# Performance work log

Measured on AMD Instinct MI355X. Metric: run time of the kernel, lower is better.

The kernel has to match this reference:

```python
import jax, jax.numpy as jnp
import numpy as np


def setup_inputs() -> dict:
    key = jax.random.key(0)
    ks = jax.random.split(key, 4)
    B, C, H, W = 4, 512, 64, 64
    A = 512  # attention_dim
    x = jax.random.normal(ks[0], (B, C, H, W), dtype=jnp.float32)
    # 1x1 conv weights as [out_ch, in_ch] matrices (kaiming-like scale)
    scale = np.sqrt(2.0 / C).astype(np.float32)
    Wq = jax.random.normal(ks[1], (A, C), dtype=jnp.float32) * scale
    Wk = jax.random.normal(ks[2], (A, C), dtype=jnp.float32) * scale
    Wv = jax.random.normal(ks[3], (C, C), dtype=jnp.float32) * scale
    bq = jnp.zeros((A,), dtype=jnp.float32)
    bk = jnp.zeros((A,), dtype=jnp.float32)
    bv = jnp.zeros((C,), dtype=jnp.float32)
    return {"x": x, "Wq": Wq, "bq": bq, "Wk": Wk, "bk": bk, "Wv": Wv, "bv": bv}


def reference(x, Wq, bq, Wk, bk, Wv, bv):
    B, C, H, W = x.shape
    N = H * W
    xf = x.reshape(B, C, N)  # [B, C, N]
    # 1x1 convs == per-pixel channel matmuls
    q = jnp.einsum('ac,bcn->bna', Wq, xf) + bq[None, None, :]   # [B, N, A] (query, permuted)
    k = jnp.einsum('ac,bcn->ban', Wk, xf) + bk[None, :, None]   # [B, A, N] (key)
    v = jnp.einsum('oc,bcn->bno', Wv, xf) + bv[None, None, :]   # [B, N, C] (value, permuted)
    attn = jnp.einsum('bna,bam->bnm', q, k)                     # [B, N, N]
    attn = jax.nn.softmax(attn, axis=-2)                        # softmax over dim=-2 (queries)
    out = jnp.einsum('bnm,bmc->bnc', attn, v)                   # [B, N, C]
    # Faithful to torch: .view(B, C, H, W) reinterprets the [B, N, C] buffer
    out = out.reshape(B, C, H, W)
    return x + 0.1 * out
```

## Files before the change

kernel.cpp:

```cpp
#include <hip/hip_runtime.h>
#include <stdint.h>


#define LDT 40
#define SUB 5120

typedef _Float16 f16x8 __attribute__((ext_vector_type(8)));
typedef float f32x4 __attribute__((ext_vector_type(4)));

template <int ASRC, int EPI, int NSUB>
__global__ void __launch_bounds__(256, 2) gemm_f16(
    const _Float16* __restrict__ Ap, long lda, long zsa,
    const _Float16* __restrict__ Bp, long ldb, long zsb,
    int kslice,
    const _Float16* __restrict__ fs16, long zsl,
    float* __restrict__ outF, _Float16* __restrict__ outH, long ldc, long zso,
    const float* __restrict__ bias0, const float* __restrict__ bias1,
    const float* __restrict__ xadd,
    float* __restrict__ pmax, float* __restrict__ psum, long zsp,
    float alpha)
{
  __shared__ _Float16 smem[2 * NSUB * SUB];

  const int z = blockIdx.z;
  const long i0 = (long)blockIdx.x * 128;
  const long j0 = (long)blockIdx.y * 128;
  const int t = (int)threadIdx.x;
  const int lane = t & 63;
  const int wv = t >> 6;
  const int quad = lane >> 4;
  const int lrow = lane & 15;
  const int wm = (wv & 1) << 6;
  const int wn = (wv >> 1) << 6;

  const int r0 = t >> 2;
  const int s0 = (t & 3) << 3;

  const _Float16* gA0 = Ap + z * zsa + (i0 + r0) * lda + s0;
  const _Float16* gA1 = gA0 + 64 * lda;
  const _Float16* gB0 = Bp + z * zsb + (j0 + r0) * ldb + s0;
  const _Float16* gB1 = gB0 + 64 * ldb;
  const int la0 = r0 * LDT + s0;
  const int la1 = (r0 + 64) * LDT + s0;

  const _Float16* fsZ = nullptr;
  if constexpr (ASRC == 1)
    fsZ = fs16 + z * zsl + (long)blockIdx.x * 4096 + s0;

  f32x4 acc[4][4];
  const f32x4 fz = {0.f, 0.f, 0.f, 0.f};
#pragma unroll
  for (int a = 0; a < 4; a++)
#pragma unroll
    for (int b = 0; b < 4; b++) acc[a][b] = fz;

  for (int kk = 0; kk < kslice; kk += 32 * NSUB) {
    f16x8 va[NSUB][2], vb[NSUB][2];
#pragma unroll
    for (int s = 0; s < NSUB; s++) {
      va[s][0] = *(const f16x8*)(gA0 + kk + 32 * s);
      va[s][1] = *(const f16x8*)(gA1 + kk + 32 * s);
      vb[s][0] = *(const f16x8*)(gB0 + kk + 32 * s);
      vb[s][1] = *(const f16x8*)(gB1 + kk + 32 * s);
    }
    if constexpr (ASRC == 1) {
#pragma unroll
      for (int s = 0; s < NSUB; s++) {
        const f16x8 fsv = *(const f16x8*)(fsZ + kk + 32 * s);
        va[s][0] = va[s][0] * fsv;
        va[s][1] = va[s][1] * fsv;
      }
    }
    __syncthreads();
#pragma unroll
    for (int s = 0; s < NSUB; s++) {
      *(f16x8*)&smem[s * SUB + la0] = va[s][0];
      *(f16x8*)&smem[s * SUB + la1] = va[s][1];
      *(f16x8*)&smem[(NSUB + s) * SUB + la0] = vb[s][0];
      *(f16x8*)&smem[(NSUB + s) * SUB + la1] = vb[s][1];
    }
    __syncthreads();

#pragma unroll
    for (int h = 0; h < NSUB; h++) {
      const _Float16* pA = smem + h * SUB;
      const _Float16* pB = smem + (NSUB + h) * SUB;
      f16x8 fa[4], fb[4];
#pragma unroll
      for (int f = 0; f < 4; f++) {
        fa[f] = *(const f16x8*)&pA[(wm + f * 16 + lrow) * LDT + quad * 8];
        fb[f] = *(const f16x8*)&pB[(wn + f * 16 + lrow) * LDT + quad * 8];
      }
#pragma unroll
      for (int fm = 0; fm < 4; fm++)
#pragma unroll
        for (int fn = 0; fn < 4; fn++)
          acc[fm][fn] = __builtin_amdgcn_mfma_f32_16x16x32_f16(fa[fm], fb[fn], acc[fm][fn], 0, 0, 0);
    }
  }

  const long obase = (long)z * zso;

  if constexpr (EPI == 1 || EPI == 2) {
#pragma unroll
    for (int fm = 0; fm < 4; fm++) {
      const long gi0 = i0 + wm + fm * 16 + quad * 4;
#pragma unroll
      for (int fn = 0; fn < 4; fn++) {
        const long gj = j0 + wn + fn * 16 + lrow;
        float badd = 0.f;
        if constexpr (EPI == 1) badd = (gj < 512) ? bias0[gj] : bias1[gj - 512];
#pragma unroll
        for (int r = 0; r < 4; r++) {
          float v = acc[fm][fn][r];
          if constexpr (EPI == 1) v += badd;
          else v += bias0[gi0 + r];
          outH[obase + (gi0 + r) * ldc + gj] = (_Float16)v;
        }
      }
    }
  } else if constexpr (EPI == 3) {
#pragma unroll
    for (int fm = 0; fm < 4; fm++) {
      const long gi0 = i0 + wm + fm * 16 + quad * 4;
#pragma unroll
      for (int fn = 0; fn < 4; fn++) {
        const long gj = j0 + wn + fn * 16 + lrow;
#pragma unroll
        for (int r = 0; r < 4; r++) {
          const long o = obase + (gi0 + r) * ldc + gj;
          outF[o] = fmaf(alpha, acc[fm][fn][r], xadd[o]);
        }
      }
    }
  } else {
    __syncthreads();
    float* Ls = (float*)smem;
#pragma unroll
    for (int fn = 0; fn < 4; fn++) {
      float mx = -3.4e38f;
#pragma unroll
      for (int fm = 0; fm < 4; fm++)
#pragma unroll
        for (int r = 0; r < 4; r++) mx = fmaxf(mx, acc[fm][fn][r]);
      Ls[(wv * 4 + quad) * 64 + fn * 16 + lrow] = mx;
    }
    __syncthreads();
    {
      const int c = t & 127;
      const int h = t >> 7;
      const int wvv = ((c >> 6) << 1) + h;
      const int wc = c & 63;
      float M = -3.4e38f;
#pragma unroll
      for (int q = 0; q < 4; q++) M = fmaxf(M, Ls[(wvv * 4 + q) * 64 + wc]);
      Ls[1024 + h * 128 + c] = M;
    }
    __syncthreads();
    if (t < 128) {
      float Mcol = fmaxf(Ls[1024 + t], Ls[1152 + t]);
      pmax[z * zsp + (long)blockIdx.x * 4096 + j0 + t] = Mcol;
      Ls[1280 + t] = Mcol;
    }
    __syncthreads();
#pragma unroll
    for (int fn = 0; fn < 4; fn++) {
      const int colc = wn + fn * 16 + lrow;
      const float Mcol = Ls[1280 + colc];
      const long gj = j0 + colc;
      float sm = 0.f;
#pragma unroll
      for (int fm = 0; fm < 4; fm++) {
        const long gi0 = i0 + wm + fm * 16 + quad * 4;
#pragma unroll
        for (int r = 0; r < 4; r++) {
          float e = __expf(acc[fm][fn][r] - Mcol);
          sm += e;
          outH[obase + (gi0 + r) * ldc + gj] = (_Float16)e;
        }
      }
      Ls[(wv * 4 + quad) * 64 + fn * 16 + lrow] = sm;
    }
    __syncthreads();
    if (t < 128) {
      const int wc = t & 63;
      const int ch = t >> 6;
      float s = 0.f;
#pragma unroll
      for (int h = 0; h < 2; h++) {
        const int wvv = (ch << 1) + h;
#pragma unroll
        for (int q = 0; q < 4; q++) s += Ls[(wvv * 4 + q) * 64 + wc];
      }
      psum[z * zsp + (long)blockIdx.x * 4096 + j0 + t] = s;
    }
  }
}

__global__ void convert_weights(const float* __restrict__ Wq, const float* __restrict__ Wk,
                                const float* __restrict__ Wv,
                                _Float16* __restrict__ WQK, _Float16* __restrict__ Wv16)
{
  int idx = blockIdx.x * 256 + threadIdx.x;
  if (idx < 524288)
    WQK[idx] = (_Float16)((idx < 262144) ? Wq[idx] : Wk[idx - 262144]);
  else
    Wv16[idx - 524288] = (_Float16)Wv[idx - 524288];
}

__global__ void transpose_x(const float* __restrict__ x, _Float16* __restrict__ xT)
{
  __shared__ float tile[32][33];
  const int b = blockIdx.z;
  const int n0 = blockIdx.x * 32;
  const int c0 = blockIdx.y * 32;
  const int tx = threadIdx.x;
  const int ty = threadIdx.y;
  const float* xb = x + (long)b * 2097152;
#pragma unroll
  for (int k = 0; k < 4; k++)
    tile[ty + k * 8][tx] = xb[(long)(c0 + ty + k * 8) * 4096 + n0 + tx];
  __syncthreads();
  _Float16* xTb = xT + (long)b * 2097152;
#pragma unroll
  for (int k = 0; k < 4; k++)
    xTb[(long)(n0 + ty + k * 8) * 512 + c0 + tx] = (_Float16)tile[tx][ty + k * 8];
}

__global__ void stats_scale(const float* __restrict__ pmax, const float* __restrict__ psum,
                            _Float16* __restrict__ fs16)
{
  const int idx = blockIdx.x * 256 + threadIdx.x;
  const int z = idx >> 12;
  const int m = idx & 4095;
  const float* pm = pmax + (long)z * 131072 + m;
  const float* ps = psum + (long)z * 131072 + m;
  float M = -3.4e38f, S = 0.f;
  for (int i = 0; i < 32; i++) {
    float m2 = pm[(long)i * 4096], s2 = ps[(long)i * 4096];
    float nm = fmaxf(M, m2);
    S = S * __expf(M - nm) + s2 * __expf(m2 - nm);
    M = nm;
  }
  const float lse = M + __logf(S);
  _Float16* fo = fs16 + (long)z * 131072 + m;
  for (int i = 0; i < 32; i++)
    fo[(long)i * 4096] = (_Float16)__expf(pm[(long)i * 4096] - lse);
}

extern "C" void kernel_launch(void* const* d_in, const int* in_sizes, int n_in,
                              void* d_out, int out_size, void* d_ws, size_t ws_size,
                              hipStream_t stream)
{
  const float* x  = (const float*)d_in[0];
  const float* Wq = (const float*)d_in[1];
  const float* bq = (const float*)d_in[2];
  const float* Wk = (const float*)d_in[3];
  const float* bk = (const float*)d_in[4];
  const float* Wv = (const float*)d_in[5];
  const float* bv = (const float*)d_in[6];
  float* out = (float*)d_out;

  char* w = (char*)d_ws;
  _Float16* WQK   = (_Float16*)(w + 0);
  _Float16* Wv16  = (_Float16*)(w + 1048576);
  _Float16* xT    = (_Float16*)(w + 1572864);
  _Float16* QK    = (_Float16*)(w + 18350080);
  _Float16* Vt    = (_Float16*)(w + 51904512);
  float*    pmaxB = (float*)   (w + 68747264);
  float*    psumB = (float*)   (w + 70844416);
  _Float16* fs16  = (_Float16*)(w + 72941568);
  _Float16* S16   = (_Float16*)(w + 75038720);

  convert_weights<<<3072, 256, 0, stream>>>(Wq, Wk, Wv, WQK, Wv16);
  transpose_x<<<dim3(128, 16, 4), dim3(32, 8), 0, stream>>>(x, xT);

  gemm_f16<0, 1, 2><<<dim3(32, 8, 4), 256, 0, stream>>>(
      xT, 512, 2097152L, WQK, 512, 0L, 512, nullptr, 0L,
      nullptr, QK, 1024, 4194304L, bq, bk, nullptr, nullptr, nullptr, 0L, 0.f);
  gemm_f16<0, 2, 2><<<dim3(4, 32, 4), 256, 0, stream>>>(
      Wv16, 512, 0L, xT, 512, 2097152L, 512, nullptr, 0L,
      nullptr, Vt, 4096, 2097152L, bv, nullptr, nullptr, nullptr, nullptr, 0L, 0.f);
  gemm_f16<0, 4, 2><<<dim3(32, 32, 4), 256, 0, stream>>>(
      QK, 1024, 4194304L, QK + 512, 1024, 4194304L, 512, nullptr, 0L,
      nullptr, S16, 4096, 16777216L, nullptr, nullptr, nullptr,
      pmaxB, psumB, 131072L, 0.f);
  stats_scale<<<64, 256, 0, stream>>>(pmaxB, psumB, fs16);
  gemm_f16<1, 3, 4><<<dim3(32, 4, 4), 256, 0, stream>>>(
      S16, 4096, 16777216L, Vt, 4096, 2097152L, 4096, fs16, 131072L,
      out, nullptr, 512, 2097152L, nullptr, nullptr, x, nullptr, nullptr, 0L, 0.1f);
}
```

Baseline: 317.9 us.

## Prefetch next K-chunk into registers during MFMA and remap load thread indexing

For NSUB>=4 the GEMM loop now issues the global loads for the next K chunk into registers before running the MFMAs on the current shared-memory chunk, so memory latency overlaps compute. The fs scaling multiply moves to store time, and the global-load thread-to-row/column mapping is changed so each group of 16 lanes covers 16 rows. The cost is more live registers, which may reduce occupancy under the (256,2) launch bounds.

Result: slower. 437.5 us (+37.6%).

```diff
diff --git a/kernel.cpp b/kernel.cpp
--- a/kernel.cpp
+++ b/kernel.cpp
@@ -33,8 +33,8 @@
   const int wm = (wv & 1) << 6;
   const int wn = (wv >> 1) << 6;
 
-  const int r0 = t >> 2;
-  const int s0 = (t & 3) << 3;
+  const int r0 = ((t >> 6) << 4) | (t & 15);
+  const int s0 = ((t >> 4) & 3) << 3;
 
   const _Float16* gA0 = Ap + z * zsa + (i0 + r0) * lda + s0;
   const _Float16* gA1 = gA0 + 64 * lda;
@@ -54,33 +54,33 @@
 #pragma unroll
     for (int b = 0; b < 4; b++) acc[a][b] = fz;
 
-  for (int kk = 0; kk < kslice; kk += 32 * NSUB) {
-    f16x8 va[NSUB][2], vb[NSUB][2];
+  f16x8 va[NSUB][2], vb[NSUB][2], vf[NSUB];
+
+  auto loadChunk = [&](int kk) {
 #pragma unroll
     for (int s = 0; s < NSUB; s++) {
       va[s][0] = *(const f16x8*)(gA0 + kk + 32 * s);
       va[s][1] = *(const f16x8*)(gA1 + kk + 32 * s);
       vb[s][0] = *(const f16x8*)(gB0 + kk + 32 * s);
       vb[s][1] = *(const f16x8*)(gB1 + kk + 32 * s);
-    }
-    if constexpr (ASRC == 1) {
-#pragma unroll
-      for (int s = 0; s < NSUB; s++) {
-        const f16x8 fsv = *(const f16x8*)(fsZ + kk + 32 * s);
-        va[s][0] = va[s][0] * fsv;
-        va[s][1] = va[s][1] * fsv;
-      }
-    }
-    __syncthreads();
+      if constexpr (ASRC == 1) vf[s] = *(const f16x8*)(fsZ + kk + 32 * s);
+    }
+  };
+  auto storeChunk = [&]() {
 #pragma unroll
     for (int s = 0; s < NSUB; s++) {
-      *(f16x8*)&smem[s * SUB + la0] = va[s][0];
-      *(f16x8*)&smem[s * SUB + la1] = va[s][1];
+      f16x8 a0 = va[s][0], a1 = va[s][1];
+      if constexpr (ASRC == 1) {
+        a0 = a0 * vf[s];
+        a1 = a1 * vf[s];
+      }
+      *(f16x8*)&smem[s * SUB + la0] = a0;
+      *(f16x8*)&smem[s * SUB + la1] = a1;
       *(f16x8*)&smem[(NSUB + s) * SUB + la0] = vb[s][0];
       *(f16x8*)&smem[(NSUB + s) * SUB + la1] = vb[s][1];
     }
-    __syncthreads();
-
+  };
+  auto mfmaChunk = [&]() {
 #pragma unroll
     for (int h = 0; h < NSUB; h++) {
       const _Float16* pA = smem + h * SUB;
@@ -96,6 +96,26 @@
 #pragma unroll
         for (int fn = 0; fn < 4; fn++)
           acc[fm][fn] = __builtin_amdgcn_mfma_f32_16x16x32_f16(fa[fm], fb[fn], acc[fm][fn], 0, 0, 0);
+    }
+  };
+
+  constexpr int KSTEP = 32 * NSUB;
+  if constexpr (NSUB >= 4) {
+    loadChunk(0);
+    for (int kk = 0; kk < kslice; kk += KSTEP) {
+      __syncthreads();
+      storeChunk();
+      __syncthreads();
+      if (kk + KSTEP < kslice) loadChunk(kk + KSTEP);
+      mfmaChunk();
+    }
+  } else {
+    for (int kk = 0; kk < kslice; kk += KSTEP) {
+      loadChunk(kk);
+      __syncthreads();
+      storeChunk();
+      __syncthreads();
+      mfmaChunk();
     }
   }
 
```

## Double-buffer final attention GEMM with direct global-to-LDS async loads and swizzled layout

Applied to the files above, without the earlier changes.

Adds a second mainloop variant that copies A/B tiles straight from global memory into LDS through global_load_lds, double-buffered so the next k-step loads while MFMAs run on the current one. The LDS layout becomes an XOR-swizzled 32-wide row in place of padded rows to avoid bank conflicts, and the softmax column scale now multiplies the A fragments after they are read from LDS. Only the final S·V GEMM uses it, with NSUB lowered from 4 to 2. The goal is to hide global latency and remove the register round trip, at the cost of more LDS per block and per-fragment multiplies.

New measurement: 325.4 us. 2.4% more time.

```diff
diff --git a/kernel.cpp b/kernel.cpp
--- a/kernel.cpp
+++ b/kernel.cpp
@@ -8,7 +8,14 @@
 typedef _Float16 f16x8 __attribute__((ext_vector_type(8)));
 typedef float f32x4 __attribute__((ext_vector_type(4)));
 
-template <int ASRC, int EPI, int NSUB>
+__device__ __forceinline__ void async16(const _Float16* g, _Float16* l)
+{
+  __builtin_amdgcn_global_load_lds(
+      (const __attribute__((address_space(1))) void*)g,
+      (__attribute__((address_space(3))) void*)l, 16, 0, 0);
+}
+
+template <int ASRC, int EPI, int NSUB, int STG>
 __global__ void __launch_bounds__(256, 2) gemm_f16(
     const _Float16* __restrict__ Ap, long lda, long zsa,
     const _Float16* __restrict__ Bp, long ldb, long zsb,
@@ -20,7 +27,8 @@
     float* __restrict__ pmax, float* __restrict__ psum, long zsp,
     float alpha)
 {
-  __shared__ _Float16 smem[2 * NSUB * SUB];
+  constexpr int SMEM_E = (STG == 1) ? (4 * NSUB * 4096) : (2 * NSUB * SUB);
+  __shared__ _Float16 smem[SMEM_E];
 
   const int z = blockIdx.z;
   const long i0 = (long)blockIdx.x * 128;
@@ -33,20 +41,6 @@
   const int wm = (wv & 1) << 6;
   const int wn = (wv >> 1) << 6;
 
-  const int r0 = t >> 2;
-  const int s0 = (t & 3) << 3;
-
-  const _Float16* gA0 = Ap + z * zsa + (i0 + r0) * lda + s0;
-  const _Float16* gA1 = gA0 + 64 * lda;
-  const _Float16* gB0 = Bp + z * zsb + (j0 + r0) * ldb + s0;
-  const _Float16* gB1 = gB0 + 64 * ldb;
-  const int la0 = r0 * LDT + s0;
-  const int la1 = (r0 + 64) * LDT + s0;
-
-  const _Float16* fsZ = nullptr;
-  if constexpr (ASRC == 1)
-    fsZ = fs16 + z * zsl + (long)blockIdx.x * 4096 + s0;
-
   f32x4 acc[4][4];
   const f32x4 fz = {0.f, 0.f, 0.f, 0.f};
 #pragma unroll
@@ -54,48 +48,130 @@
 #pragma unroll
     for (int b = 0; b < 4; b++) acc[a][b] = fz;
 
-  for (int kk = 0; kk < kslice; kk += 32 * NSUB) {
-    f16x8 va[NSUB][2], vb[NSUB][2];
-#pragma unroll
-    for (int s = 0; s < NSUB; s++) {
-      va[s][0] = *(const f16x8*)(gA0 + kk + 32 * s);
-      va[s][1] = *(const f16x8*)(gA1 + kk + 32 * s);
-      vb[s][0] = *(const f16x8*)(gB0 + kk + 32 * s);
-      vb[s][1] = *(const f16x8*)(gB1 + kk + 32 * s);
-    }
-    if constexpr (ASRC == 1) {
+  if constexpr (STG == 0) {
+    const int r0 = t >> 2;
+    const int s0 = (t & 3) << 3;
+
+    const _Float16* gA0 = Ap + z * zsa + (i0 + r0) * lda + s0;
+    const _Float16* gA1 = gA0 + 64 * lda;
+    const _Float16* gB0 = Bp + z * zsb + (j0 + r0) * ldb + s0;
+    const _Float16* gB1 = gB0 + 64 * ldb;
+    const int la0 = r0 * LDT + s0;
+    const int la1 = (r0 + 64) * LDT + s0;
+
+    const _Float16* fsZ = nullptr;
+    if constexpr (ASRC == 1)
+      fsZ = fs16 + z * zsl + (long)blockIdx.x * 4096 + s0;
+
+    for (int kk = 0; kk < kslice; kk += 32 * NSUB) {
+      f16x8 va[NSUB][2], vb[NSUB][2];
 #pragma unroll
       for (int s = 0; s < NSUB; s++) {
-        const f16x8 fsv = *(const f16x8*)(fsZ + kk + 32 * s);
-        va[s][0] = va[s][0] * fsv;
-        va[s][1] = va[s][1] * fsv;
-      }
-    }
-    __syncthreads();
-#pragma unroll
-    for (int s = 0; s < NSUB; s++) {
-      *(f16x8*)&smem[s * SUB + la0] = va[s][0];
-      *(f16x8*)&smem[s * SUB + la1] = va[s][1];
-      *(f16x8*)&smem[(NSUB + s) * SUB + la0] = vb[s][0];
-      *(f16x8*)&smem[(NSUB + s) * SUB + la1] = vb[s][1];
-    }
-    __syncthreads();
-
-#pragma unroll
-    for (int h = 0; h < NSUB; h++) {
-      const _Float16* pA = smem + h * SUB;
-      const _Float16* pB = smem + (NSUB + h) * SUB;
-      f16x8 fa[4], fb[4];
-#pragma unroll
-      for (int f = 0; f < 4; f++) {
-        fa[f] = *(const f16x8*)&pA[(wm + f * 16 + lrow) * LDT + quad * 8];
-        fb[f] = *(const f16x8*)&pB[(wn + f * 16 + lrow) * LDT + quad * 8];
-      }
-#pragma unroll
-      for (int fm = 0; fm < 4; fm++)
-#pragma unroll
-        for (int fn = 0; fn < 4; fn++)
-          acc[fm][fn] = __builtin_amdgcn_mfma_f32_16x16x32_f16(fa[fm], fb[fn], acc[fm][fn], 0, 0, 0);
+        va[s][0] = *(const f16x8*)(gA0 + kk + 32 * s);
+        va[s][1] = *(const f16x8*)(gA1 + kk + 32 * s);
+        vb[s][0] = *(const f16x8*)(gB0 + kk + 32 * s);
+        vb[s][1] = *(const f16x8*)(gB1 + kk + 32 * s);
+      }
+      if constexpr (ASRC == 1) {
+#pragma unroll
+        for (int s = 0; s < NSUB; s++) {
+          const f16x8 fsv = *(const f16x8*)(fsZ + kk + 32 * s);
+          va[s][0] = va[s][0] * fsv;
+          va[s][1] = va[s][1] * fsv;
+        }
+      }
+      __syncthreads();
+#pragma unroll
+      for (int s = 0; s < NSUB; s++) {
+        *(f16x8*)&smem[s * SUB + la0] = va[s][0];
+        *(f16x8*)&smem[s * SUB + la1] = va[s][1];
+        *(f16x8*)&smem[(NSUB + s) * SUB + la0] = vb[s][0];
+        *(f16x8*)&smem[(NSUB + s) * SUB + la1] = vb[s][1];
+      }
+      __syncthreads();
+
+#pragma unroll
+      for (int h = 0; h < NSUB; h++) {
+        const _Float16* pA = smem + h * SUB;
+        const _Float16* pB = smem + (NSUB + h) * SUB;
+        f16x8 fa[4], fb[4];
+#pragma unroll
+        for (int f = 0; f < 4; f++) {
+          fa[f] = *(const f16x8*)&pA[(wm + f * 16 + lrow) * LDT + quad * 8];
+          fb[f] = *(const f16x8*)&pB[(wn + f * 16 + lrow) * LDT + quad * 8];
+        }
+#pragma unroll
+        for (int fm = 0; fm < 4; fm++)
+#pragma unroll
+          for (int fn = 0; fn < 4; fn++)
+            acc[fm][fn] = __builtin_amdgcn_mfma_f32_16x16x32_f16(fa[fm], fb[fn], acc[fm][fn], 0, 0, 0);
+      }
+    }
+  } else {
+    constexpr int KSTEP = 32 * NSUB;
+    constexpr int BUFE = 2 * NSUB * 4096;
+    const int crow = lane >> 2;
+    const int ks8 = (((lane & 3) ^ ((lane >> 3) & 3)) << 3);
+
+    const _Float16* gAc0 = Ap + z * zsa + (i0 + 16 * wv + crow) * lda + ks8;
+    const _Float16* gAc1 = gAc0 + 64 * lda;
+    const _Float16* gBc0 = Bp + z * zsb + (j0 + 16 * wv + crow) * ldb + ks8;
+    const _Float16* gBc1 = gBc0 + 64 * ldb;
+    _Float16* ldsC0 = smem + wv * 512;
+    _Float16* ldsC1 = smem + (wv + 4) * 512;
+
+    const _Float16* fsZq = nullptr;
+    if constexpr (ASRC == 1)
+      fsZq = fs16 + z * zsl + (long)blockIdx.x * 4096 + quad * 8;
+
+    const int qs = ((quad ^ ((lrow >> 1) & 3)) << 3);
+
+    auto stage = [&](int buf, int kk) {
+#pragma unroll
+      for (int s = 0; s < NSUB; s++) {
+        const int ab = buf * BUFE + s * 4096;
+        const int bb = buf * BUFE + (NSUB + s) * 4096;
+        async16(gAc0 + kk + 32 * s, ldsC0 + ab);
+        async16(gAc1 + kk + 32 * s, ldsC1 + ab);
+        async16(gBc0 + kk + 32 * s, ldsC0 + bb);
+        async16(gBc1 + kk + 32 * s, ldsC1 + bb);
+      }
+    };
+
+    stage(0, 0);
+    __syncthreads();
+    int cur = 0;
+    for (int kk = 0; kk < kslice; kk += KSTEP) {
+      f16x8 fsv[NSUB];
+      if constexpr (ASRC == 1) {
+#pragma unroll
+        for (int h = 0; h < NSUB; h++)
+          fsv[h] = *(const f16x8*)(fsZq + kk + 32 * h);
+        __builtin_amdgcn_sched_barrier(0);
+      }
+      if (kk + KSTEP < kslice) stage(cur ^ 1, kk + KSTEP);
+#pragma unroll
+      for (int h = 0; h < NSUB; h++) {
+        const _Float16* pA = smem + cur * BUFE + h * 4096;
+        const _Float16* pB = smem + cur * BUFE + (NSUB + h) * 4096;
+        f16x8 fa[4], fb[4];
+#pragma unroll
+        for (int f = 0; f < 4; f++) {
+          fa[f] = *(const f16x8*)&pA[(wm + f * 16 + lrow) * 32 + qs];
+          fb[f] = *(const f16x8*)&pB[(wn + f * 16 + lrow) * 32 + qs];
+        }
+        if constexpr (ASRC == 1) {
+#pragma unroll
+          for (int f = 0; f < 4; f++) fa[f] = fa[f] * fsv[h];
+        }
+#pragma unroll
+        for (int fm = 0; fm < 4; fm++)
+#pragma unroll
+          for (int fn = 0; fn < 4; fn++)
+            acc[fm][fn] = __builtin_amdgcn_mfma_f32_16x16x32_f16(fa[fm], fb[fn], acc[fm][fn], 0, 0, 0);
+      }
+      __syncthreads();
+      cur ^= 1;
     }
   }
 
@@ -275,18 +351,18 @@
   convert_weights<<<3072, 256, 0, stream>>>(Wq, Wk, Wv, WQK, Wv16);
   transpose_x<<<dim3(128, 16, 4), dim3(32, 8), 0, stream>>>(x, xT);
 
-  gemm_f16<0, 1, 2><<<dim3(32, 8, 4), 256, 0, stream>>>(
+  gemm_f16<0, 1, 2, 0><<<dim3(32, 8, 4), 256, 0, stream>>>(
       xT, 512, 2097152L, WQK, 512, 0L, 512, nullptr, 0L,
       nullptr, QK, 1024, 4194304L, bq, bk, nullptr, nullptr, nullptr, 0L, 0.f);
-  gemm_f16<0, 2, 2><<<dim3(4, 32, 4), 256, 0, stream>>>(
+  gemm_f16<0, 2, 2, 0><<<dim3(4, 32, 4), 256, 0, stream>>>(
       Wv16, 512, 0L, xT, 512, 2097152L, 512, nullptr, 0L,
       nullptr, Vt, 4096, 2097152L, bv, nullptr, nullptr, nullptr, nullptr, 0L, 0.f);
-  gemm_f16<0, 4, 2><<<dim3(32, 32, 4), 256, 0, stream>>>(
+  gemm_f16<0, 4, 2, 0><<<dim3(32, 32, 4), 256, 0, stream>>>(
       QK, 1024, 4194304L, QK + 512, 1024, 4194304L, 512, nullptr, 0L,
       nullptr, S16, 4096, 16777216L, nullptr, nullptr, nullptr,
       pmaxB, psumB, 131072L, 0.f);
   stats_scale<<<64, 256, 0, stream>>>(pmaxB, psumB, fs16);
-  gemm_f16<1, 3, 4><<<dim3(32, 4, 4), 256, 0, stream>>>(
+  gemm_f16<1, 3, 2, 1><<<dim3(32, 4, 4), 256, 0, stream>>>(
       S16, 4096, 16777216L, Vt, 4096, 2097152L, 4096, fs16, 131072L,
       out, nullptr, 512, 2097152L, nullptr, nullptr, x, nullptr, nullptr, 0L, 0.1f);
 }
```
